# Kernel tuning notes

Measured on AMD Instinct MI355X. Metric: run time of the kernel, lower is better.

## Reference

```python
import jax, jax.numpy as jnp
import numpy as np

B, T, C, H = 4, 2048, 1024, 16
HD = C // H  # head dim = 64


def setup_inputs() -> dict:
    key = jax.random.key(0)
    ks = jax.random.split(key, 5)
    s = 1.0 / np.sqrt(C)
    return {
        "x": jax.random.normal(ks[0], (B, T, C), jnp.float32),
        "Wk": jax.random.normal(ks[1], (C, C), jnp.float32) * s,
        "bk": jnp.zeros((C,), jnp.float32),
        "Wq": jax.random.normal(ks[2], (C, C), jnp.float32) * s,
        "bq": jnp.zeros((C,), jnp.float32),
        "Wv": jax.random.normal(ks[3], (C, C), jnp.float32) * s,
        "bv": jnp.zeros((C,), jnp.float32),
        "Wp": jax.random.normal(ks[4], (C, C), jnp.float32) * s,
        "bp": jnp.zeros((C,), jnp.float32),
    }


def reference(x, Wk, bk, Wq, bq, Wv, bv, Wp, bp):
    # Linear(in, out): y = x @ W.T + b  (W stored as [out, in], torch convention)
    k = (x @ Wk.T + bk).reshape(B, T, H, HD).transpose(0, 2, 1, 3)  # [B,H,T,HD]
    q = (x @ Wq.T + bq).reshape(B, T, H, HD).transpose(0, 2, 1, 3)
    v = (x @ Wv.T + bv).reshape(B, T, H, HD).transpose(0, 2, 1, 3)
    scale = 1.0 / np.sqrt(HD)
    att = jnp.einsum("bhqd,bhkd->bhqk", q, k) * scale  # [B,H,T,T]
    causal = jnp.tril(jnp.ones((T, T), bool))
    att = jnp.where(causal[None, None, :, :], att, -jnp.inf)
    att = jax.nn.softmax(att, axis=-1)
    y = jnp.einsum("bhqk,bhkd->bhqd", att, v)  # [B,H,T,HD]
    y = y.transpose(0, 2, 1, 3).reshape(B, T, C)
    return y @ Wp.T + bp
```

## Files before the change

kernel.cpp:

```cpp
#include <hip/hip_runtime.h>
#include <hip/hip_bf16.h>
#include <cmath>

#define Tt 2048
#define Cc 1024
#define Hh 16
#define HDd 64

typedef __attribute__((ext_vector_type(8))) short short8;
typedef __attribute__((ext_vector_type(4))) float f32x4;

#define ASYNC16(gp, lp)                                       \
    __builtin_amdgcn_global_load_lds(                         \
        (const __attribute__((address_space(1))) void*)(gp),  \
        (__attribute__((address_space(3))) void*)(lp), 16, 0, 0)

__device__ __forceinline__ unsigned short f32_bf16(float f) {
    unsigned u = __float_as_uint(f);
    u += 0x7FFF + ((u >> 16) & 1);
    return (unsigned short)(u >> 16);
}
__device__ __forceinline__ unsigned short f32_bf16_rn(float f) {
    return (unsigned short)((__float_as_uint(f) + 0x8000u) >> 16);
}
__device__ __forceinline__ float fast_exp2(float x) {
#if __has_builtin(__builtin_amdgcn_exp2f)
    return __builtin_amdgcn_exp2f(x);
#else
    return exp2f(x);
#endif
}

__global__ __launch_bounds__(256) void cvt_all(
    const float* __restrict__ x, const float* __restrict__ a,
    const float* __restrict__ b, const float* __restrict__ c,
    const float* __restrict__ d, unsigned short* __restrict__ ox,
    unsigned short* __restrict__ oa, unsigned short* __restrict__ ob,
    unsigned short* __restrict__ oc, unsigned short* __restrict__ od) {
    const int id = blockIdx.x * 256 + threadIdx.x;
    const float* src; unsigned short* dst; int sub;
    if (id < 2097152) {
        src = x; dst = ox; sub = id;
    } else {
        const int wi = id - 2097152;
        const int which = wi >> 18;
        sub = wi & 262143;
        if (which == 0)      { src = a; dst = oa; }
        else if (which == 1) { src = b; dst = ob; }
        else if (which == 2) { src = c; dst = oc; }
        else                 { src = d; dst = od; }
    }
    float4 v = ((const float4*)src)[sub];
    ushort4 o;
    o.x = f32_bf16(v.x); o.y = f32_bf16(v.y);
    o.z = f32_bf16(v.z); o.w = f32_bf16(v.w);
    ((ushort4*)dst)[sub] = o;
}

__global__ __launch_bounds__(512, 2) void gemm_qkv8(
    const unsigned short* __restrict__ A,
    const unsigned short* __restrict__ Wcat,
    const float* __restrict__ bq, const float* __restrict__ bk,
    const float* __restrict__ bv,
    unsigned short* __restrict__ qout, unsigned short* __restrict__ kout,
    unsigned short* __restrict__ vout) {
    extern __shared__ unsigned short lds[];

    const int tid  = threadIdx.x;
    const int wid  = tid >> 6;
    const int lane = tid & 63;
    const int quad = lane >> 4;
    const int lr   = lane & 15;
    const int wr   = wid >> 2;
    const int wc   = wid & 3;

    const int bm0 = blockIdx.y * 256;
    const int bn0 = blockIdx.x * 256;

    const int srow  = wid * 8 + (lane >> 3);
    const int scol  = ((lane & 7) ^ (lane >> 3)) * 8;
    const int sldso = wid * 512;

    const int a_r   = wr * 64 + lr;
    const int b_r   = wc * 32 + lr;
    const int slot0 = (quad ^ (lr & 7)) * 8;
    const int slot1 = ((quad ^ 4) ^ (lr & 7)) * 8;

    f32x4 acc[8][4];
    const f32x4 zero = {0.f, 0.f, 0.f, 0.f};
#pragma unroll
    for (int i = 0; i < 8; ++i)
#pragma unroll
        for (int j = 0; j < 4; ++j) acc[i][j] = zero;

    short8 areg[4][2];
    short8 breg[2][2][2];

#define STG(S, BUF, REG, GB, GROW)                                          \
    do {                                                                    \
        if ((S) < 16) {                                                     \
            unsigned short* lb = lds + ((BUF) * 4 + (REG)) * 8192 + sldso;  \
            const unsigned short* gp =                                      \
                (GB) + (size_t)((GROW) + srow) * Cc + (S) * 64 + scol;      \
            ASYNC16(gp, lb);                                                \
            ASYNC16(gp + (size_t)64 * Cc, lb + 4096);                       \
        }                                                                   \
    } while (0)

#define LDA(mh)                                                             \
    do {                                                                    \
        const unsigned short* ab = bufb + (mh) * 8192;                      \
        _Pragma("unroll") for (int mf = 0; mf < 4; ++mf) {                  \
            areg[mf][0] = *(const short8*)(ab + (a_r + mf * 16) * 64 + slot0); \
            areg[mf][1] = *(const short8*)(ab + (a_r + mf * 16) * 64 + slot1); \
        }                                                                   \
    } while (0)

#define LDB(nh)                                                             \
    do {                                                                    \
        const unsigned short* bb = bufb + (2 + (nh)) * 8192;                \
        _Pragma("unroll") for (int nf = 0; nf < 2; ++nf) {                  \
            breg[nh][nf][0] = *(const short8*)(bb + (b_r + nf * 16) * 64 + slot0); \
            breg[nh][nf][1] = *(const short8*)(bb + (b_r + nf * 16) * 64 + slot1); \
        }                                                                   \
    } while (0)

#define MFMA_PHASE(mh, nh)                                                  \
    _Pragma("unroll") for (int mf = 0; mf < 4; ++mf)                        \
    _Pragma("unroll") for (int nf = 0; nf < 2; ++nf) {                      \
        acc[(mh)*4+mf][(nh)*2+nf] = __builtin_amdgcn_mfma_f32_16x16x32_bf16( \
            areg[mf][0], breg[nh][nf][0], acc[(mh)*4+mf][(nh)*2+nf], 0,0,0); \
        acc[(mh)*4+mf][(nh)*2+nf] = __builtin_amdgcn_mfma_f32_16x16x32_bf16( \
            areg[mf][1], breg[nh][nf][1], acc[(mh)*4+mf][(nh)*2+nf], 0,0,0); \
    }

#define TILE(T, BC, WN)                                                     \
    {                                                                       \
        const unsigned short* bufb = lds + (BC) * 32768;                    \
        LDA(0);                                                             \
        LDB(0);                                                             \
        STG((T) + 1, (BC) ^ 1, 1, A, bm0 + 128);                            \
        __builtin_amdgcn_s_barrier();                                       \
        asm volatile("s_waitcnt lgkmcnt(0)" ::: "memory");                  \
        __builtin_amdgcn_s_setprio(1);                                      \
        MFMA_PHASE(0, 0);                                                   \
        __builtin_amdgcn_s_setprio(0);                                      \
        __builtin_amdgcn_s_barrier();                                       \
        LDB(1);                                                             \
        STG((T) + 1, (BC) ^ 1, 3, Wcat, bn0 + 128);                         \
        __builtin_amdgcn_s_barrier();                                       \
        asm volatile("s_waitcnt lgkmcnt(0)" ::: "memory");                  \
        __builtin_amdgcn_s_setprio(1);                                      \
        MFMA_PHASE(0, 1);                                                   \
        __builtin_amdgcn_s_setprio(0);                                      \
        __builtin_amdgcn_s_barrier();                                       \
        LDA(1);                                                             \
        STG((T) + 2, (BC), 0, A, bm0);                                      \
        __builtin_amdgcn_s_barrier();                                       \
        asm volatile("s_waitcnt lgkmcnt(0)" ::: "memory");                  \
        __builtin_amdgcn_s_setprio(1);                                      \
        MFMA_PHASE(1, 0);                                                   \
        __builtin_amdgcn_s_setprio(0);                                      \
        __builtin_amdgcn_s_barrier();                                       \
        STG((T) + 2, (BC), 2, Wcat, bn0);                                   \
        __builtin_amdgcn_s_barrier();                                       \
        __builtin_amdgcn_s_setprio(1);                                      \
        MFMA_PHASE(1, 1);                                                   \
        __builtin_amdgcn_s_setprio(0);                                      \
        asm volatile("s_waitcnt vmcnt(" #WN ")" ::: "memory");              \
        __builtin_amdgcn_s_barrier();                                       \
    }

    STG(0, 0, 0, A, bm0);
    STG(0, 0, 1, A, bm0 + 128);
    STG(0, 0, 2, Wcat, bn0);
    STG(0, 0, 3, Wcat, bn0 + 128);
    STG(1, 1, 0, A, bm0);
    STG(1, 1, 2, Wcat, bn0);
    asm volatile("s_waitcnt vmcnt(4)" ::: "memory");
    __builtin_amdgcn_s_barrier();

    for (int t2 = 0; t2 < 7; ++t2) {
        const int T0 = t2 * 2;
        TILE(T0, 0, 4);
        TILE(T0 + 1, 1, 4);
    }
    TILE(14, 0, 0);
    TILE(15, 1, 0);

#undef TILE
#undef MFMA_PHASE
#undef LDB
#undef LDA
#undef STG

    const int which = bn0 >> 10;
    const float* bias = (which == 0) ? bq : (which == 1) ? bk : bv;
    unsigned short* outp = (which == 0) ? qout : (which == 1) ? kout : vout;
    const float scale = (which == 0) ? 0.1803368801111204f : 1.0f;
    const bool vmode = (which == 2);
    const int nb = bn0 & 1023;

#pragma unroll
    for (int nh = 0; nh < 2; ++nh)
#pragma unroll
        for (int nf = 0; nf < 2; ++nf) {
            const int nl = nb + nh * 128 + wc * 32 + nf * 16 + lr;
            const float bvv = bias[nl];
            const int h = nl >> 6, hd = nl & 63;
#pragma unroll
            for (int mh = 0; mh < 2; ++mh)
#pragma unroll
                for (int mf = 0; mf < 4; ++mf) {
                    const f32x4 a = acc[mh * 4 + mf][nh * 2 + nf];
                    const int m0 = bm0 + mh * 128 + wr * 64 + mf * 16 + quad * 4;
                    const int b = m0 >> 11, t0 = m0 & 2047;
                    if (vmode) {
                        ushort4 pk;
                        pk.x = f32_bf16_rn(a[0] + bvv);
                        pk.y = f32_bf16_rn(a[1] + bvv);
                        pk.z = f32_bf16_rn(a[2] + bvv);
                        pk.w = f32_bf16_rn(a[3] + bvv);
                        *(ushort4*)(outp + (((size_t)(b * Hh + h)) * HDd + hd) * Tt + t0) = pk;
                    } else {
#pragma unroll
                        for (int r = 0; r < 4; ++r) {
                            outp[(((size_t)(b * Hh + h)) * Tt + t0 + r) * HDd + hd] =
                                f32_bf16_rn((a[r] + bvv) * scale);
                        }
                    }
                }
        }
}

__global__ __launch_bounds__(256) void gemm_proj(const unsigned short* __restrict__ A,
                                                 const unsigned short* __restrict__ W,
                                                 const float* __restrict__ bias,
                                                 float* __restrict__ out) {
    __shared__ unsigned short sA[2][128 * 32];
    __shared__ unsigned short sB[2][64 * 32];

    const int tid  = threadIdx.x;
    const int bm0  = blockIdx.y * 128;
    const int bn0  = blockIdx.x * 64;
    const int wid  = tid >> 6;
    const int lane = tid & 63;
    const int quad = lane >> 4;
    const int lr   = lane & 15;
    const int wm   = (wid & 1) * 64;
    const int wn   = (wid >> 1) * 32;

    const int sr   = lane >> 2;
    const int scol = (lane & 3) * 8;
    const int row0 = wid * 16 + sr;
    const int row1 = 64 + wid * 16 + sr;
    const int lo0  = wid * 512;
    const int lo1  = (4 + wid) * 512;

    f32x4 acc[4][2];
    f32x4 zero = {0.f, 0.f, 0.f, 0.f};
#pragma unroll
    for (int i = 0; i < 4; i++)
#pragma unroll
        for (int j = 0; j < 2; j++) acc[i][j] = zero;

    ASYNC16(A + (size_t)(bm0 + row0) * Cc + scol, sA[0] + lo0);
    ASYNC16(A + (size_t)(bm0 + row1) * Cc + scol, sA[0] + lo1);
    ASYNC16(W + (size_t)(bn0 + row0) * Cc + scol, sB[0] + lo0);
    __syncthreads();

    for (int kt = 0; kt < Cc / 32; ++kt) {
        const int cur = kt & 1, nxt = cur ^ 1;
        if (kt + 1 < Cc / 32) {
            const int kb = (kt + 1) * 32;
            ASYNC16(A + (size_t)(bm0 + row0) * Cc + kb + scol, sA[nxt] + lo0);
            ASYNC16(A + (size_t)(bm0 + row1) * Cc + kb + scol, sA[nxt] + lo1);
            ASYNC16(W + (size_t)(bn0 + row0) * Cc + kb + scol, sB[nxt] + lo0);
        }

        short8 af[4], bf[2];
#pragma unroll
        for (int i = 0; i < 4; i++)
            af[i] = *(const short8*)(sA[cur] + (wm + i * 16 + lr) * 32 + quad * 8);
#pragma unroll
        for (int j = 0; j < 2; j++)
            bf[j] = *(const short8*)(sB[cur] + (wn + j * 16 + lr) * 32 + quad * 8);
#pragma unroll
        for (int i = 0; i < 4; i++)
#pragma unroll
            for (int j = 0; j < 2; j++)
                acc[i][j] = __builtin_amdgcn_mfma_f32_16x16x32_bf16(af[i], bf[j], acc[i][j], 0, 0, 0);

        __syncthreads();
    }

#pragma unroll
    for (int j = 0; j < 2; j++) {
        const int n = bn0 + wn + j * 16 + lr;
        const float bvv = bias[n];
#pragma unroll
        for (int i = 0; i < 4; i++)
#pragma unroll
            for (int r = 0; r < 4; r++) {
                const int m = bm0 + wm + i * 16 + quad * 4 + r;
                out[(size_t)m * Cc + n] = acc[i][j][r] + bvv;
            }
    }
}

__global__ __launch_bounds__(256, 4) void attn(const unsigned short* __restrict__ q,
                                               const unsigned short* __restrict__ k,
                                               const unsigned short* __restrict__ vt,
                                               unsigned short* __restrict__ y) {
    __shared__ unsigned short sK[2][64 * 64];
    __shared__ unsigned short sV[2][64 * 64];
    __shared__ unsigned short sP[4][16 * 64];

    const int tid  = threadIdx.x;
    const int wid  = tid >> 6;
    const int lane = tid & 63;
    const int quad = lane >> 4;
    const int lr   = lane & 15;

    const int bh = blockIdx.x;
    const int qx = blockIdx.y;
    const size_t headq = (size_t)bh * Tt * HDd;
    const unsigned short* kg = k + headq;
    const unsigned short* vg = vt + headq;
    const int b = bh >> 4, h = bh & 15;

    const int g_r = lane >> 3;
    const int g_c = ((lane & 7) ^ g_r) * 8;
    const unsigned short* kst = kg + (size_t)(wid * 16 + g_r) * HDd + g_c;
    const unsigned short* vst = vg + (size_t)(wid * 16 + g_r) * Tt + g_c;
    unsigned short* dK0 = sK[0] + wid * 1024;
    unsigned short* dK1 = sK[1] + wid * 1024;
    unsigned short* dV0 = sV[0] + wid * 1024;
    unsigned short* dV1 = sV[1] + wid * 1024;

#define STAGE_KV(BUF, KB)                                                   \
    do {                                                                    \
        unsigned short* dK = (BUF) ? dK1 : dK0;                             \
        unsigned short* dV = (BUF) ? dV1 : dV0;                             \
        ASYNC16(kst + (size_t)(KB) * HDd,       dK);                        \
        ASYNC16(kst + (size_t)((KB) + 8) * HDd, dK + 512);                  \
        ASYNC16(vst + (KB),                     dV);                        \
        ASYNC16(vst + (size_t)8 * Tt + (KB),    dV + 512);                  \
    } while (0)

    const int fr_off = lr * 64 + ((quad ^ (lr & 7)) * 8);
    const int hq8 = (((lr >> 3) ^ ((quad & 1) << 2)) * 8);
    const int pwb = quad * 256 + (lr & 7);
    unsigned short* sPw = sP[wid];

    const f32x4 zero = {0.f, 0.f, 0.f, 0.f};

    for (int pass = 0; pass < 2; ++pass) {
        const int qt = pass ? (31 - qx) : qx;
        const int qb = qt * 64;
        const int ntiles = qt + 1;

        const unsigned short* qp = q + headq + (size_t)(qb + wid * 16 + lr) * HDd;
        const short8 qf0 = *(const short8*)(qp + quad * 8);
        const short8 qf1 = *(const short8*)(qp + 32 + quad * 8);

        f32x4 o[4];
        float l_run[4];
#pragma unroll
        for (int i = 0; i < 4; i++) { o[i] = zero; l_run[i] = 0.f; }

        STAGE_KV(0, 0);
        __syncthreads();

        for (int kt = 0; kt < ntiles; ++kt) {
            const int cur = kt & 1;
            if (kt + 1 < ntiles) STAGE_KV(cur ^ 1, (kt + 1) * 64);

            const unsigned short* bK = sK[cur];
            const unsigned short* bV = sV[cur];

            short8 kf[4][2];
#pragma unroll
            for (int nt = 0; nt < 4; nt++) {
                kf[nt][0] = *(const short8*)(bK + nt * 1024 + fr_off);
                kf[nt][1] = *(const short8*)(bK + nt * 1024 + (fr_off ^ 32));
            }

            f32x4 sc[4];
            __builtin_amdgcn_s_setprio(1);
#pragma unroll
            for (int nt = 0; nt < 4; nt++) {
                f32x4 a = __builtin_amdgcn_mfma_f32_16x16x32_bf16(qf0, kf[nt][0], zero, 0, 0, 0);
                sc[nt]  = __builtin_amdgcn_mfma_f32_16x16x32_bf16(qf1, kf[nt][1], a, 0, 0, 0);
            }
            __builtin_amdgcn_s_setprio(0);

            short8 vf[4][2];
#pragma unroll
            for (int nt = 0; nt < 4; nt++) {
                vf[nt][0] = *(const short8*)(bV + nt * 1024 + fr_off);
                vf[nt][1] = *(const short8*)(bV + nt * 1024 + (fr_off ^ 32));
            }

            if (kt == qt) {
#pragma unroll
                for (int nt = 0; nt < 4; nt++)
#pragma unroll
                    for (int r = 0; r < 4; r++)
                        sc[nt][r] = (nt * 16 + lr <= wid * 16 + quad * 4 + r)
                                        ? sc[nt][r] : -INFINITY;
            }

#pragma unroll
            for (int nt = 0; nt < 4; nt++)
#pragma unroll
                for (int r = 0; r < 4; r++) {
                    const float p = fast_exp2(sc[nt][r]);
                    l_run[r] += p;
                    sPw[pwb + r * 64 + ((nt * 16 ^ r * 8) ^ hq8)] = f32_bf16_rn(p);
                }

            const short8 pa0 = *(const short8*)(sPw + fr_off);
            const short8 pa1 = *(const short8*)(sPw + (fr_off ^ 32));

            __builtin_amdgcn_s_setprio(1);
#pragma unroll
            for (int nt = 0; nt < 4; nt++) {
                o[nt] = __builtin_amdgcn_mfma_f32_16x16x32_bf16(pa0, vf[nt][0], o[nt], 0, 0, 0);
                o[nt] = __builtin_amdgcn_mfma_f32_16x16x32_bf16(pa1, vf[nt][1], o[nt], 0, 0, 0);
            }
            __builtin_amdgcn_s_setprio(0);

            __syncthreads();
        }

#pragma unroll
        for (int r = 0; r < 4; r++) {
            float ls = l_run[r];
            ls += __shfl_xor(ls, 1);
            ls += __shfl_xor(ls, 2);
            ls += __shfl_xor(ls, 4);
            ls += __shfl_xor(ls, 8);
            const float inv = 1.0f / ls;
            const int t = qb + wid * 16 + quad * 4 + r;
#pragma unroll
            for (int nt = 0; nt < 4; nt++) {
                const int dim = nt * 16 + lr;
                y[((size_t)(b * Tt + t)) * Cc + h * HDd + dim] =
                    f32_bf16_rn(o[nt][r] * inv);
            }
        }
    }
#undef STAGE_KV
}

extern "C" void kernel_launch(void* const* d_in, const int* in_sizes, int n_in,
                              void* d_out, int out_size, void* d_ws, size_t ws_size,
                              hipStream_t stream) {
    const float* x  = (const float*)d_in[0];
    const float* Wk = (const float*)d_in[1];
    const float* bk = (const float*)d_in[2];
    const float* Wq = (const float*)d_in[3];
    const float* bq = (const float*)d_in[4];
    const float* Wv = (const float*)d_in[5];
    const float* bv = (const float*)d_in[6];
    const float* Wp = (const float*)d_in[7];
    const float* bp = (const float*)d_in[8];
    float* out = (float*)d_out;

    char* ws = (char*)d_ws;
    size_t off = 0;
    auto alloc = [&](size_t bytes) { char* p = ws + off; off += bytes; return p; };
    const size_t MK = (size_t)8192 * 1024;
    const size_t NK = (size_t)1024 * 1024;
    unsigned short* xb   = (unsigned short*)alloc(MK * 2);
    unsigned short* Wcat = (unsigned short*)alloc(3 * NK * 2);
    unsigned short* Wqb  = Wcat;
    unsigned short* Wkb  = Wcat + NK;
    unsigned short* Wvb  = Wcat + 2 * NK;
    unsigned short* Wpb  = (unsigned short*)alloc(NK * 2);
    unsigned short* qh   = (unsigned short*)alloc(MK * 2);
    unsigned short* kh   = (unsigned short*)alloc(MK * 2);
    unsigned short* vth  = (unsigned short*)alloc(MK * 2);
    unsigned short* ya   = (unsigned short*)alloc(MK * 2);

    static bool lds_attr_set = false;
    if (!lds_attr_set) {
        (void)hipFuncSetAttribute((const void*)gemm_qkv8,
                                  hipFuncAttributeMaxDynamicSharedMemorySize,
                                  131072);
        lds_attr_set = true;
    }

    cvt_all<<<12288, 256, 0, stream>>>(x, Wq, Wk, Wv, Wp, xb, Wqb, Wkb, Wvb, Wpb);

    gemm_qkv8<<<dim3(12, 32), 512, 131072, stream>>>(xb, Wcat, bq, bk, bv, qh, kh, vth);

    attn<<<dim3(64, 16), 256, 0, stream>>>(qh, kh, vth, ya);

    gemm_proj<<<dim3(16, 64), 256, 0, stream>>>(ya, Wpb, bp, out);
}
```

Measured before the change: 259.3 us.

## Replace projection GEMM with 256x128 eight-wave pipelined kernel and XCD-aware block swizzle

```diff
diff --git a/kernel.cpp b/kernel.cpp
--- a/kernel.cpp
+++ b/kernel.cpp
@@ -74,8 +74,16 @@
     const int wr   = wid >> 2;
     const int wc   = wid & 3;
 
-    const int bm0 = blockIdx.y * 256;
-    const int bn0 = blockIdx.x * 256;
+    const int id   = blockIdx.y * 12 + blockIdx.x;
+    const int xcd  = id & 7;
+    const int rank = id >> 3;
+    const int ls   = rank >> 4;
+    const int w    = rank & 15;
+    const int sID  = ls * 8 + xcd;
+    const int by   = (sID / 3) * 4 + (w >> 2);
+    const int bx   = (sID % 3) * 4 + (w & 3);
+    const int bm0  = by * 256;
+    const int bn0  = bx * 256;
 
     const int srow  = wid * 8 + (lane >> 3);
     const int scol  = ((lane & 7) ^ (lane >> 3)) * 8;
@@ -233,77 +241,159 @@
         }
 }
 
-__global__ __launch_bounds__(256) void gemm_proj(const unsigned short* __restrict__ A,
-                                                 const unsigned short* __restrict__ W,
-                                                 const float* __restrict__ bias,
-                                                 float* __restrict__ out) {
-    __shared__ unsigned short sA[2][128 * 32];
-    __shared__ unsigned short sB[2][64 * 32];
+__global__ __launch_bounds__(512, 2) void gemm_proj8(
+    const unsigned short* __restrict__ A,
+    const unsigned short* __restrict__ W,
+    const float* __restrict__ bias,
+    float* __restrict__ out) {
+    extern __shared__ unsigned short lds[];
 
     const int tid  = threadIdx.x;
-    const int bm0  = blockIdx.y * 128;
-    const int bn0  = blockIdx.x * 64;
     const int wid  = tid >> 6;
     const int lane = tid & 63;
     const int quad = lane >> 4;
     const int lr   = lane & 15;
-    const int wm   = (wid & 1) * 64;
-    const int wn   = (wid >> 1) * 32;
-
-    const int sr   = lane >> 2;
-    const int scol = (lane & 3) * 8;
-    const int row0 = wid * 16 + sr;
-    const int row1 = 64 + wid * 16 + sr;
-    const int lo0  = wid * 512;
-    const int lo1  = (4 + wid) * 512;
-
-    f32x4 acc[4][2];
-    f32x4 zero = {0.f, 0.f, 0.f, 0.f};
-#pragma unroll
-    for (int i = 0; i < 4; i++)
-#pragma unroll
-        for (int j = 0; j < 2; j++) acc[i][j] = zero;
-
-    ASYNC16(A + (size_t)(bm0 + row0) * Cc + scol, sA[0] + lo0);
-    ASYNC16(A + (size_t)(bm0 + row1) * Cc + scol, sA[0] + lo1);
-    ASYNC16(W + (size_t)(bn0 + row0) * Cc + scol, sB[0] + lo0);
-    __syncthreads();
-
-    for (int kt = 0; kt < Cc / 32; ++kt) {
-        const int cur = kt & 1, nxt = cur ^ 1;
-        if (kt + 1 < Cc / 32) {
-            const int kb = (kt + 1) * 32;
-            ASYNC16(A + (size_t)(bm0 + row0) * Cc + kb + scol, sA[nxt] + lo0);
-            ASYNC16(A + (size_t)(bm0 + row1) * Cc + kb + scol, sA[nxt] + lo1);
-            ASYNC16(W + (size_t)(bn0 + row0) * Cc + kb + scol, sB[nxt] + lo0);
-        }
-
-        short8 af[4], bf[2];
-#pragma unroll
-        for (int i = 0; i < 4; i++)
-            af[i] = *(const short8*)(sA[cur] + (wm + i * 16 + lr) * 32 + quad * 8);
-#pragma unroll
-        for (int j = 0; j < 2; j++)
-            bf[j] = *(const short8*)(sB[cur] + (wn + j * 16 + lr) * 32 + quad * 8);
-#pragma unroll
-        for (int i = 0; i < 4; i++)
-#pragma unroll
-            for (int j = 0; j < 2; j++)
-                acc[i][j] = __builtin_amdgcn_mfma_f32_16x16x32_bf16(af[i], bf[j], acc[i][j], 0, 0, 0);
-
-        __syncthreads();
-    }
-
-#pragma unroll
-    for (int j = 0; j < 2; j++) {
-        const int n = bn0 + wn + j * 16 + lr;
+    const int wr   = wid >> 2;
+    const int wc   = wid & 3;
+
+    const int id   = blockIdx.y * 8 + blockIdx.x;
+    const int xcd  = id & 7;
+    const int rank = id >> 3;
+    const int by   = xcd * 4 + (rank >> 3);
+    const int bx   = rank & 7;
+    const int bm0  = by * 256;
+    const int bn0  = bx * 128;
+
+    const int srow  = wid * 8 + (lane >> 3);
+    const int scol  = ((lane & 7) ^ (lane >> 3)) * 8;
+    const int sldso = wid * 512;
+
+    const int a_r   = wr * 64 + lr;
+    const int b_r2  = (wc & 1) * 32 + lr;
+    const int breg_off = 16384 + (wc >> 1) * 4096;
+    const int slot0 = (quad ^ (lr & 7)) * 8;
+    const int slot1 = ((quad ^ 4) ^ (lr & 7)) * 8;
+
+    f32x4 acc[8][2];
+    const f32x4 zero = {0.f, 0.f, 0.f, 0.f};
+#pragma unroll
+    for (int i = 0; i < 8; ++i)
+#pragma unroll
+        for (int j = 0; j < 2; ++j) acc[i][j] = zero;
+
+    short8 areg[4][2];
+    short8 breg[2][2];
+
+#define STGA(S, BUF, REG_OFF, GROW)                                         \
+    do {                                                                    \
+        if ((S) < 16) {                                                     \
+            unsigned short* lb = lds + (BUF) * 24576 + (REG_OFF) + sldso;   \
+            const unsigned short* gp =                                      \
+                A + (size_t)(bm0 + (GROW) + srow) * Cc + (S) * 64 + scol;   \
+            ASYNC16(gp, lb);                                                \
+            ASYNC16(gp + (size_t)64 * Cc, lb + 4096);                       \
+        }                                                                   \
+    } while (0)
+
+#define STGB(S, BUF, REG_OFF, NROW)                                         \
+    do {                                                                    \
+        if ((S) < 16) {                                                     \
+            unsigned short* lb = lds + (BUF) * 24576 + (REG_OFF) + sldso;   \
+            const unsigned short* gp =                                      \
+                W + (size_t)(bn0 + (NROW) + srow) * Cc + (S) * 64 + scol;   \
+            ASYNC16(gp, lb);                                                \
+        }                                                                   \
+    } while (0)
+
+#define LDA_P(mh)                                                           \
+    do {                                                                    \
+        const unsigned short* ab = bufb + (mh) * 8192;                      \
+        _Pragma("unroll") for (int mf = 0; mf < 4; ++mf) {                  \
+            areg[mf][0] = *(const short8*)(ab + (a_r + mf * 16) * 64 + slot0); \
+            areg[mf][1] = *(const short8*)(ab + (a_r + mf * 16) * 64 + slot1); \
+        }                                                                   \
+    } while (0)
+
+#define LDB_P                                                               \
+    do {                                                                    \
+        const unsigned short* bb = bufb + breg_off;                         \
+        _Pragma("unroll") for (int nf = 0; nf < 2; ++nf) {                  \
+            breg[nf][0] = *(const short8*)(bb + (b_r2 + nf * 16) * 64 + slot0); \
+            breg[nf][1] = *(const short8*)(bb + (b_r2 + nf * 16) * 64 + slot1); \
+        }                                                                   \
+    } while (0)
+
+#define MFMA_P(mh)                                                          \
+    _Pragma("unroll") for (int mf = 0; mf < 4; ++mf)                        \
+    _Pragma("unroll") for (int nf = 0; nf < 2; ++nf) {                      \
+        acc[(mh)*4+mf][nf] = __builtin_amdgcn_mfma_f32_16x16x32_bf16(       \
+            areg[mf][0], breg[nf][0], acc[(mh)*4+mf][nf], 0, 0, 0);         \
+        acc[(mh)*4+mf][nf] = __builtin_amdgcn_mfma_f32_16x16x32_bf16(       \
+            areg[mf][1], breg[nf][1], acc[(mh)*4+mf][nf], 0, 0, 0);         \
+    }
+
+#define TILE_P(T, BC, WN)                                                   \
+    {                                                                       \
+        const unsigned short* bufb = lds + (BC) * 24576;                    \
+        LDA_P(0);                                                           \
+        LDB_P;                                                              \
+        STGA((T) + 1, (BC) ^ 1, 8192, 128);                                 \
+        STGB((T) + 1, (BC) ^ 1, 20480, 64);                                 \
+        __builtin_amdgcn_s_barrier();                                       \
+        asm volatile("s_waitcnt lgkmcnt(0)" ::: "memory");                  \
+        __builtin_amdgcn_s_setprio(1);                                      \
+        MFMA_P(0);                                                          \
+        __builtin_amdgcn_s_setprio(0);                                      \
+        __builtin_amdgcn_s_barrier();                                       \
+        LDA_P(1);                                                           \
+        STGA((T) + 2, (BC), 0, 0);                                          \
+        STGB((T) + 2, (BC), 16384, 0);                                      \
+        __builtin_amdgcn_s_barrier();                                       \
+        asm volatile("s_waitcnt lgkmcnt(0)" ::: "memory");                  \
+        __builtin_amdgcn_s_setprio(1);                                      \
+        MFMA_P(1);                                                          \
+        __builtin_amdgcn_s_setprio(0);                                      \
+        asm volatile("s_waitcnt vmcnt(" #WN ")" ::: "memory");              \
+        __builtin_amdgcn_s_barrier();                                       \
+    }
+
+    STGA(0, 0, 0, 0);
+    STGA(0, 0, 8192, 128);
+    STGB(0, 0, 16384, 0);
+    STGB(0, 0, 20480, 64);
+    STGA(1, 1, 0, 0);
+    STGB(1, 1, 16384, 0);
+    asm volatile("s_waitcnt vmcnt(3)" ::: "memory");
+    __builtin_amdgcn_s_barrier();
+
+    for (int t2 = 0; t2 < 7; ++t2) {
+        const int T0 = t2 * 2;
+        TILE_P(T0, 0, 3);
+        TILE_P(T0 + 1, 1, 3);
+    }
+    TILE_P(14, 0, 0);
+    TILE_P(15, 1, 0);
+
+#undef TILE_P
+#undef MFMA_P
+#undef LDB_P
+#undef LDA_P
+#undef STGB
+#undef STGA
+
+#pragma unroll
+    for (int nf = 0; nf < 2; ++nf) {
+        const int n = bn0 + wc * 32 + nf * 16 + lr;
         const float bvv = bias[n];
 #pragma unroll
-        for (int i = 0; i < 4; i++)
-#pragma unroll
-            for (int r = 0; r < 4; r++) {
-                const int m = bm0 + wm + i * 16 + quad * 4 + r;
-                out[(size_t)m * Cc + n] = acc[i][j][r] + bvv;
+        for (int mh = 0; mh < 2; ++mh)
+#pragma unroll
+            for (int mf = 0; mf < 4; ++mf) {
+                const f32x4 a = acc[mh * 4 + mf][nf];
+                const int m0 = bm0 + mh * 128 + wr * 64 + mf * 16 + quad * 4;
+#pragma unroll
+                for (int r = 0; r < 4; ++r)
+                    out[(size_t)(m0 + r) * Cc + n] = a[r] + bvv;
             }
     }
 }
@@ -489,6 +579,9 @@
         (void)hipFuncSetAttribute((const void*)gemm_qkv8,
                                   hipFuncAttributeMaxDynamicSharedMemorySize,
                                   131072);
+        (void)hipFuncSetAttribute((const void*)gemm_proj8,
+                                  hipFuncAttributeMaxDynamicSharedMemorySize,
+                                  98304);
         lds_attr_set = true;
     }
 
@@ -498,5 +591,5 @@
 
     attn<<<dim3(64, 16), 256, 0, stream>>>(qh, kh, vth, ya);
 
-    gemm_proj<<<dim3(16, 64), 256, 0, stream>>>(ya, Wpb, bp, out);
-}
+    gemm_proj8<<<dim3(8, 32), 512, 98304, stream>>>(ya, Wpb, bp, out);
+}
```

Result: faster. 247.0 us (-4.8%).
